# Optimization experiments

Measured on AMD Instinct MI355X. Metric: run time of the kernel, lower is better.

The kernel has to match this reference:

```python
import jax, jax.numpy as jnp
import numpy as np

N_NODES = 50000
N_EDGES = 800000
IN_DIM = 128
OUT_DIM = 64
HEADS = 8
HEAD_DIM = OUT_DIM // HEADS
NEG_SLOPE = 0.2


def setup_inputs() -> dict:
    key = jax.random.key(0)
    k1, k2, k3, k4, k5 = jax.random.split(key, 5)
    x = jax.random.normal(k1, (N_NODES, IN_DIM), dtype=jnp.float32)
    edge_indices = jax.random.randint(k2, (2, N_EDGES), 0, N_NODES, dtype=jnp.int64)
    # Linear(input_dim, output_dim, bias=False): weight is [out, in]
    W = jax.random.normal(k3, (OUT_DIM, IN_DIM), dtype=jnp.float32) * (1.0 / np.sqrt(IN_DIM))
    src_attn = jax.random.normal(k4, (HEADS, HEAD_DIM), dtype=jnp.float32) * (1.0 / np.sqrt(HEAD_DIM))
    dst_attn = jax.random.normal(k5, (HEADS, HEAD_DIM), dtype=jnp.float32) * (1.0 / np.sqrt(HEAD_DIM))
    return {"x": x, "edge_indices": edge_indices, "W": W, "src_attn": src_attn, "dst_attn": dst_attn}


def reference(x, edge_indices, W, src_attn, dst_attn):
    # Eval mode: all dropouts are identity.
    N = x.shape[0]
    # add self loops
    loops = jnp.arange(N, dtype=edge_indices.dtype)
    ei = jnp.concatenate([edge_indices, jnp.stack([loops, loops])], axis=1)  # [2, E+N]
    row, col = ei[0], ei[1]

    h = (x @ W.T).reshape(N, HEADS, HEAD_DIM)  # [N, H, D]
    s = jnp.einsum("nhd,hd->nh", h, src_attn)  # [N, H]
    d = jnp.einsum("nhd,hd->nh", h, dst_attn)  # [N, H]

    e = jax.nn.leaky_relu(s[row] + d[col], negative_slope=NEG_SLOPE)  # [E', H]

    # segment softmax over rows (torch.sparse.softmax with dim=1 normalizes per row)
    m = jax.ops.segment_max(e, row, num_segments=N)          # [N, H]
    ex = jnp.exp(e - m[row])                                 # [E', H]
    denom = jax.ops.segment_sum(ex, row, num_segments=N)    # [N, H]
    w = ex / denom[row]                                      # [E', H]

    # sparse.mm per head: out[row] += w * h[col]
    msg = w[:, :, None] * h[col]                             # [E', H, D]
    out = jax.ops.segment_sum(msg, row, num_segments=N)      # [N, H, D]
    return out.reshape(N, HEADS * HEAD_DIM)
```

## Files before the change

kernel.cpp:

```cpp
#include <hip/hip_runtime.h>

#define NN 50000
#define NEG_SLOPE 0.2f
#define LOG2E 1.44269504088896340736f

#define GEMM_NB ((NN + 63) / 64)
#define NBUCK 196
#define EPB 4096
#define CAPF 4608
#define CAPH 2816

typedef __bf16 bf16x8 __attribute__((ext_vector_type(8)));
typedef float f32x4 __attribute__((ext_vector_type(4)));

static __device__ __forceinline__ unsigned short f2bf(float f) {
    __bf16 b = (__bf16)f;
    return __builtin_bit_cast(unsigned short, b);
}
static __device__ __forceinline__ float bf2f(unsigned short u) {
    return __uint_as_float(((unsigned)u) << 16);
}

static __device__ __forceinline__ int detect_i64(const int* __restrict__ ei,
                                                 int lane) {
    unsigned long long b = __ballot(ei[2 * lane + 1] != 0);
    return (b == 0ull) ? 1 : 0;
}

__global__ __launch_bounds__(256) void k_fused0(
        const float* __restrict__ x, const float* __restrict__ W,
        const float* __restrict__ sa, const float* __restrict__ da,
        const int* __restrict__ ei,
        unsigned short* __restrict__ hb, float* __restrict__ s,
        float* __restrict__ d, int* __restrict__ S, int* __restrict__ LP,
        unsigned* __restrict__ tmp, int E, int NB1) {
    __shared__ int hist[256];
    __shared__ int pref[256];
    __shared__ unsigned lrec[EPB];
    const int tid  = threadIdx.x;
    const int lane = tid & 63;

    if (blockIdx.x >= GEMM_NB) {
        const int bx = blockIdx.x - GEMM_NB;
        hist[tid] = 0;
        const int f = detect_i64(ei, lane);
        __syncthreads();

        const int base = bx * EPB + tid * 16;
        int rw[16], cl[16];
        const bool fullvec = (base + 16 <= E) && ((E & 3) == 0);
        if (f) {
            if (fullvec) {
                const int4* p = (const int4*)(ei + 2 * base);
                const int4* q = (const int4*)(ei + 2 * E + 2 * base);
                #pragma unroll
                for (int g = 0; g < 8; ++g) {
                    int4 a = p[g]; int4 b = q[g];
                    rw[2 * g] = a.x; rw[2 * g + 1] = a.z;
                    cl[2 * g] = b.x; cl[2 * g + 1] = b.z;
                }
            } else {
                #pragma unroll
                for (int k = 0; k < 16; ++k) {
                    int e = base + k;
                    rw[k] = (e < E) ? ei[2 * e] : -1;
                    cl[k] = (e < E) ? ei[2 * E + 2 * e] : 0;
                }
            }
        } else {
            if (fullvec) {
                const int4* p = (const int4*)(ei + base);
                const int4* q = (const int4*)(ei + E + base);
                #pragma unroll
                for (int g = 0; g < 4; ++g) {
                    int4 a = p[g]; int4 b = q[g];
                    rw[4 * g] = a.x; rw[4 * g + 1] = a.y;
                    rw[4 * g + 2] = a.z; rw[4 * g + 3] = a.w;
                    cl[4 * g] = b.x; cl[4 * g + 1] = b.y;
                    cl[4 * g + 2] = b.z; cl[4 * g + 3] = b.w;
                }
            } else {
                #pragma unroll
                for (int k = 0; k < 16; ++k) {
                    int e = base + k;
                    rw[k] = (e < E) ? ei[e] : -1;
                    cl[k] = (e < E) ? ei[E + e] : 0;
                }
            }
        }

        #pragma unroll
        for (int k = 0; k < 16; ++k)
            if (rw[k] >= 0) atomicAdd(&hist[rw[k] >> 8], 1);
        __syncthreads();

        const int myCnt = hist[tid];
        pref[tid] = myCnt;
        __syncthreads();
        for (int off = 1; off < 256; off <<= 1) {
            int u = (tid >= off) ? pref[tid - off] : 0;
            __syncthreads();
            pref[tid] += u;
            __syncthreads();
        }
        if (tid < NBUCK) {
            S[tid * NB1 + bx]  = myCnt;
            LP[tid * NB1 + bx] = pref[tid] - myCnt;
        }
        hist[tid] = pref[tid] - myCnt;
        __syncthreads();

        #pragma unroll
        for (int k = 0; k < 16; ++k) {
            if (rw[k] >= 0) {
                int lp = atomicAdd(&hist[rw[k] >> 8], 1);
                lrec[lp] = ((unsigned)(rw[k] & 255) << 24) | (unsigned)cl[k];
            }
        }
        __syncthreads();

        const int tot = pref[255];
        for (int j = tid; j < tot; j += 256)
            tmp[bx * EPB + j] = lrec[j];
        return;
    }

    const int wave = tid >> 6;
    const int c    = lane & 15;
    const int kg   = lane >> 4;
    const int n0   = blockIdx.x * 64 + wave * 16;

    bf16x8 bf[4][4];
    #pragma unroll
    for (int kt = 0; kt < 4; ++kt) {
        #pragma unroll
        for (int ot = 0; ot < 4; ++ot) {
            const float* wp = &W[(ot * 16 + c) * 128 + kt * 32 + kg * 8];
            f32x4 w0 = *(const f32x4*)wp;
            f32x4 w1 = *(const f32x4*)(wp + 4);
            bf16x8 b;
            #pragma unroll
            for (int j = 0; j < 4; ++j) { b[j] = (__bf16)w0[j]; b[4 + j] = (__bf16)w1[j]; }
            bf[kt][ot] = b;
        }
    }

    int nr = n0 + c; if (nr > NN - 1) nr = NN - 1;
    const float* xp = &x[(long)nr * 128 + kg * 8];

    f32x4 acc[4] = {};
    #pragma unroll
    for (int kt = 0; kt < 4; ++kt) {
        f32x4 x0 = *(const f32x4*)(xp + kt * 32);
        f32x4 x1 = *(const f32x4*)(xp + kt * 32 + 4);
        bf16x8 a;
        #pragma unroll
        for (int j = 0; j < 4; ++j) { a[j] = (__bf16)x0[j]; a[4 + j] = (__bf16)x1[j]; }
        #pragma unroll
        for (int ot = 0; ot < 4; ++ot)
            acc[ot] = __builtin_amdgcn_mfma_f32_16x16x32_bf16(a, bf[kt][ot], acc[ot], 0, 0, 0);
    }

    float sav[4], dav[4];
    #pragma unroll
    for (int ot = 0; ot < 4; ++ot) {
        sav[ot] = sa[ot * 16 + c] * LOG2E;
        dav[ot] = da[ot * 16 + c] * LOG2E;
    }

    const int nodebase = n0 + kg * 4;
    #pragma unroll
    for (int r = 0; r < 4; ++r) {
        const int n = nodebase + r;
        const bool ok = (n < NN);
        if (ok) {
            #pragma unroll
            for (int ot = 0; ot < 4; ++ot) hb[n * 64 + ot * 16 + c] = f2bf(acc[ot][r]);
        }
        float ps[4], pd[4];
        #pragma unroll
        for (int ot = 0; ot < 4; ++ot) { ps[ot] = acc[ot][r] * sav[ot]; pd[ot] = acc[ot][r] * dav[ot]; }
        #pragma unroll
        for (int m = 1; m < 8; m <<= 1) {
            #pragma unroll
            for (int ot = 0; ot < 4; ++ot) {
                ps[ot] += __shfl_xor(ps[ot], m, 64);
                pd[ot] += __shfl_xor(pd[ot], m, 64);
            }
        }
        if (ok && (c & 7) == 0) {
            const int hbid = c >> 3;
            #pragma unroll
            for (int ot = 0; ot < 4; ++ot) {
                s[n * 8 + 2 * ot + hbid] = ps[ot];
                d[n * 8 + 2 * ot + hbid] = pd[ot];
            }
        }
    }
}

__global__ __launch_bounds__(1024) void k_bgather(
        const unsigned* __restrict__ tmp, const int* __restrict__ S,
        const int* __restrict__ LP, const unsigned short* __restrict__ hb,
        const float* __restrict__ sarr, const float* __restrict__ d,
        float* __restrict__ out, int NB1) {
    __shared__ int aux2[256];
    __shared__ int aux3[256];
    __shared__ int bins[128];
    __shared__ int pref2[128];
    __shared__ unsigned u_raw[CAPF];
    __shared__ int lcol[CAPH];

    const int t    = threadIdx.x;
    const int bkt  = blockIdx.x >> 1;
    const int half = blockIdx.x & 1;
    const int lane = t & 63;
    const int wid  = t >> 6;

    if (t < 256) {
        aux2[t] = (t < NB1) ? S[bkt * NB1 + t] : 0;
        aux3[t] = (t < NB1) ? LP[bkt * NB1 + t] : 0;
    }
    __syncthreads();
    for (int off = 1; off < 256; off <<= 1) {
        int u = 0;
        if (t < 256 && t >= off) u = aux2[t - off];
        __syncthreads();
        if (t < 256) aux2[t] += u;
        __syncthreads();
    }

    for (int bx = wid; bx < NB1; bx += 16) {
        const int dst0 = bx ? aux2[bx - 1] : 0;
        const int cbx  = aux2[bx] - dst0;
        const int src0 = bx * EPB + aux3[bx];
        for (int j = lane; j < cbx; j += 64) {
            const int dp = dst0 + j;
            if (dp < CAPF) u_raw[dp] = tmp[src0 + j];
        }
    }
    __syncthreads();
    int cnt = aux2[255]; if (cnt > CAPF) cnt = CAPF;

    if (t < 128) bins[t] = 0;
    __syncthreads();
    for (int i = t; i < cnt; i += 1024) {
        const int r8 = (int)(u_raw[i] >> 24);
        if ((r8 >> 7) == half) atomicAdd(&bins[r8 & 127], 1);
    }
    __syncthreads();
    const int bv = (t < 128) ? bins[t] : 0;
    if (t < 128) pref2[t] = bv;
    __syncthreads();
    for (int off = 1; off < 128; off <<= 1) {
        int u = 0;
        if (t < 128 && t >= off) u = pref2[t - off];
        __syncthreads();
        if (t < 128) pref2[t] += u;
        __syncthreads();
    }
    if (t < 128) bins[t] = pref2[t] - bv;
    __syncthreads();
    for (int i = t; i < cnt; i += 1024) {
        const unsigned v = u_raw[i];
        const int r8 = (int)(v >> 24);
        if ((r8 >> 7) == half) {
            const int p = atomicAdd(&bins[r8 & 127], 1);
            if (p < CAPH) lcol[p] = (int)(v & 0xFFFFu);
        }
    }
    __syncthreads();

    const int o    = lane;
    const int oh   = o >> 3;
    const int eidx = lane >> 3;
    const int h    = lane & 7;

    #pragma unroll
    for (int j = 0; j < 8; ++j) {
        const int rl = j * 16 + wid;
        const int n  = bkt * 256 + half * 128 + rl;
        if (n >= NN) continue;

        const int bgn = rl ? pref2[rl - 1] : 0;
        const int end = pref2[rl];

        const float sn_h = sarr[n * 8 + h];
        float acc  = 0.0f;
        float dsum = 0.0f;

        for (int i = bgn; i < end; i += 8) {
            const int myi  = i + eidx;
            const bool val = (myi < end);
            const int c = lcol[val ? myi : (end - 1)];
            float dv = d[c * 8 + h];
            float v = sn_h + dv;
            v = fmaxf(v, NEG_SLOPE * v);
            v = val ? v : -10000.0f;
            const float ev = __builtin_amdgcn_exp2f(v);
            dsum += ev;

            #pragma unroll
            for (int k = 0; k < 8; ++k) {
                const int   c_k = __builtin_amdgcn_readlane(c, k * 8);
                const float e_k = __shfl(ev, k * 8 + oh);
                acc += e_k * bf2f(hb[c_k * 64 + o]);
            }
        }

        dsum += __shfl_xor(dsum, 8, 64);
        dsum += __shfl_xor(dsum, 16, 64);
        dsum += __shfl_xor(dsum, 32, 64);
        float denom = __shfl(dsum, oh);

        const float sn_o = sarr[n * 8 + oh];
        const float dn_o = d[n * 8 + oh];
        float vs = sn_o + dn_o;
        vs = fmaxf(vs, NEG_SLOPE * vs);
        const float es = __builtin_amdgcn_exp2f(vs);
        denom += es;
        acc += es * bf2f(hb[n * 64 + o]);

        out[n * 64 + o] = acc / denom;
    }
}

extern "C" void kernel_launch(void* const* d_in, const int* in_sizes, int n_in,
                              void* d_out, int out_size, void* d_ws, size_t ws_size,
                              hipStream_t stream) {
    const float* x  = (const float*)d_in[0];
    const int*   ei = (const int*)d_in[1];
    const float* W  = (const float*)d_in[2];
    const float* sa = (const float*)d_in[3];
    const float* da = (const float*)d_in[4];
    float* out = (float*)d_out;
    const int E = in_sizes[1] / 2;

    int NB1 = (E + EPB - 1) / EPB;
    if (NB1 > 256) NB1 = 256;

    unsigned short* hb = (unsigned short*)d_ws;
    float* s  = (float*)(hb + NN * 64);
    float* dd = s + NN * 8;
    int* S    = (int*)(dd + NN * 8);
    int* LP   = S + NBUCK * 256;
    unsigned* tmp = (unsigned*)(LP + NBUCK * 256);

    k_fused0<<<GEMM_NB + NB1, 256, 0, stream>>>(x, W, sa, da, ei,
                                                hb, s, dd, S, LP, tmp, E, NB1);
    k_bgather<<<NBUCK * 2, 1024, 0, stream>>>(tmp, S, LP, hb, s, dd, out, NB1);
}
```

Baseline: 71.51 us.

## Binary-search bucket gather and simplify per-edge aggregation to one edge per iteration

The bucket gather loop, which assigned one wave per source block, becomes a flat loop over output slots. Each thread finds its source block by binary search over the prefix sums, which balances the copy work across threads. The aggregation loop drops the 8-edges-per-wave scheme with shuffles and readlanes. Instead every lane computes the attention weight for its own head on each edge and accumulates directly, unrolled by 4. This removes cross-lane shuffles and reductions, but each lane now does redundant exp and d loads per edge, with less memory-level parallelism per iteration.

```diff
diff --git a/kernel.cpp b/kernel.cpp
--- a/kernel.cpp
+++ b/kernel.cpp
@@ -229,18 +229,19 @@
         if (t < 256) aux2[t] += u;
         __syncthreads();
     }
-
-    for (int bx = wid; bx < NB1; bx += 16) {
-        const int dst0 = bx ? aux2[bx - 1] : 0;
-        const int cbx  = aux2[bx] - dst0;
-        const int src0 = bx * EPB + aux3[bx];
-        for (int j = lane; j < cbx; j += 64) {
-            const int dp = dst0 + j;
-            if (dp < CAPF) u_raw[dp] = tmp[src0 + j];
-        }
-    }
-    __syncthreads();
     int cnt = aux2[255]; if (cnt > CAPF) cnt = CAPF;
+
+    for (int p = t; p < cnt; p += 1024) {
+        int lo = 0, hi = 255;
+        #pragma unroll
+        for (int it = 0; it < 8; ++it) {
+            const int mid = (lo + hi) >> 1;
+            if (aux2[mid] > p) hi = mid; else lo = mid + 1;
+        }
+        const int excl = lo ? aux2[lo - 1] : 0;
+        u_raw[p] = tmp[lo * EPB + aux3[lo] + (p - excl)];
+    }
+    __syncthreads();
 
     if (t < 128) bins[t] = 0;
     __syncthreads();
@@ -271,10 +272,8 @@
     }
     __syncthreads();
 
-    const int o    = lane;
-    const int oh   = o >> 3;
-    const int eidx = lane >> 3;
-    const int h    = lane & 7;
+    const int o  = lane;
+    const int oh = o >> 3;
 
     #pragma unroll
     for (int j = 0; j < 8; ++j) {
@@ -285,43 +284,25 @@
         const int bgn = rl ? pref2[rl - 1] : 0;
         const int end = pref2[rl];
 
-        const float sn_h = sarr[n * 8 + h];
+        const float sn_o = sarr[n * 8 + oh];
+        const float dn_o = d[n * 8 + oh];
         float acc  = 0.0f;
         float dsum = 0.0f;
 
-        for (int i = bgn; i < end; i += 8) {
-            const int myi  = i + eidx;
-            const bool val = (myi < end);
-            const int c = lcol[val ? myi : (end - 1)];
-            float dv = d[c * 8 + h];
-            float v = sn_h + dv;
+        #pragma unroll 4
+        for (int i = bgn; i < end; ++i) {
+            const int c = lcol[i];
+            float v = sn_o + d[c * 8 + oh];
             v = fmaxf(v, NEG_SLOPE * v);
-            v = val ? v : -10000.0f;
             const float ev = __builtin_amdgcn_exp2f(v);
             dsum += ev;
-
-            #pragma unroll
-            for (int k = 0; k < 8; ++k) {
-                const int   c_k = __builtin_amdgcn_readlane(c, k * 8);
-                const float e_k = __shfl(ev, k * 8 + oh);
-                acc += e_k * bf2f(hb[c_k * 64 + o]);
-            }
-        }
-
-        dsum += __shfl_xor(dsum, 8, 64);
-        dsum += __shfl_xor(dsum, 16, 64);
-        dsum += __shfl_xor(dsum, 32, 64);
-        float denom = __shfl(dsum, oh);
-
-        const float sn_o = sarr[n * 8 + oh];
-        const float dn_o = d[n * 8 + oh];
+            acc += ev * bf2f(hb[c * 64 + o]);
+        }
+
         float vs = sn_o + dn_o;
         vs = fmaxf(vs, NEG_SLOPE * vs);
         const float es = __builtin_amdgcn_exp2f(vs);
-        denom += es;
-        acc += es * bf2f(hb[n * 64 + o]);
-
-        out[n * 64 + o] = acc / denom;
+        out[n * 64 + o] = (acc + es * bf2f(hb[n * 64 + o])) / (dsum + es);
     }
 }
 
```

Result: slower. 78.24 us (+9.4%).
